# Kernel optimization log

Hardware: AMD Instinct MI355X
Metric: run time of the kernel (lower is better)

Reference implementation:

```python
import jax, jax.numpy as jnp
import numpy as np

B, T, E, H = 4, 2048, 1024, 16
HS = E // H
FF = 4 * E


def _layernorm(x, g, b, eps=1e-5):
    mu = jnp.mean(x, axis=-1, keepdims=True)
    var = jnp.var(x, axis=-1, keepdims=True)
    return (x - mu) * jax.lax.rsqrt(var + eps) * g + b


def setup_inputs() -> dict:
    key = jax.random.key(0)
    ks = jax.random.split(key, 12)
    s = E ** -0.5
    return {
        "x": jax.random.normal(ks[0], (B, T, E), jnp.float32),
        "Wq": jax.random.normal(ks[1], (E, E), jnp.float32) * s,
        "Wk": jax.random.normal(ks[2], (E, E), jnp.float32) * s,
        "Wv": jax.random.normal(ks[3], (E, E), jnp.float32) * s,
        "Wp": jax.random.normal(ks[4], (E, E), jnp.float32) * s,
        "bp": jnp.zeros((E,), jnp.float32),
        "W1": jax.random.normal(ks[5], (E, FF), jnp.float32) * s,
        "b1": jnp.zeros((FF,), jnp.float32),
        "W2": jax.random.normal(ks[6], (FF, E), jnp.float32) * (FF ** -0.5),
        "b2": jnp.zeros((E,), jnp.float32),
        "g1": jnp.ones((E,), jnp.float32),
        "be1": jnp.zeros((E,), jnp.float32),
        "g2": jnp.ones((E,), jnp.float32),
        "be2": jnp.zeros((E,), jnp.float32),
    }


def reference(x, Wq, Wk, Wv, Wp, bp, W1, b1, W2, b2, g1, be1, g2, be2):
    h = _layernorm(x, g1, be1)
    # per-head projections: Wq columns laid out head-by-head (matches concat order)
    q = (h @ Wq).reshape(B, T, H, HS).transpose(0, 2, 1, 3)  # [B,H,T,hs]
    k = (h @ Wk).reshape(B, T, H, HS).transpose(0, 2, 1, 3)
    v = (h @ Wv).reshape(B, T, H, HS).transpose(0, 2, 1, 3)
    # NOTE: original scales by full embedding size C**-0.5, not head_size
    scores = jnp.einsum("bhqd,bhkd->bhqk", q, k) * (E ** -0.5)
    causal = jnp.tril(jnp.ones((T, T), bool))
    scores = jnp.where(causal, scores, -jnp.inf)
    wei = jax.nn.softmax(scores, axis=-1)
    attn = jnp.einsum("bhqk,bhkd->bhqd", wei, v)  # [B,H,T,hs]
    attn = attn.transpose(0, 2, 1, 3).reshape(B, T, E)
    x = x + attn @ Wp + bp
    h2 = _layernorm(x, g2, be2)
    ff = jax.nn.relu(h2 @ W1 + b1) @ W2 + b2
    return x + ff
```

## Files before the change

kernel.cpp:

```cpp
#include <hip/hip_runtime.h>
#include <stdint.h>

typedef unsigned short u16;
typedef short s8v __attribute__((ext_vector_type(8)));
typedef float f32x4 __attribute__((ext_vector_type(4)));

#define B_SZ 4
#define T_SEQ 2048
#define E_DIM 1024
#define H_NUM 16
#define HS 64
#define FF_DIM 4096
#define M_ROWS 8192
#define QSCALE 0.0450842200f

__device__ __forceinline__ u16 f2bf(float f) {
    unsigned int u = __builtin_bit_cast(unsigned int, f);
    u += 0x7fffu + ((u >> 16) & 1u);
    return (u16)(u >> 16);
}

__device__ __forceinline__ void async_copy16(const void* g, void* l) {
    __builtin_amdgcn_global_load_lds(
        (const __attribute__((address_space(1))) unsigned int*)g,
        (__attribute__((address_space(3))) unsigned int*)l, 16, 0, 0);
}

__global__ __launch_bounds__(256)
void transpose_cast4(const float* __restrict__ s0, const float* __restrict__ s1,
                     const float* __restrict__ s2, const float* __restrict__ s3,
                     u16* __restrict__ dqkv, u16* __restrict__ dp) {
    __shared__ float tile[32][33];
    const int zz = blockIdx.z;
    const float* src = (zz == 0) ? s0 : (zz == 1) ? s1 : (zz == 2) ? s2 : s3;
    u16* dst = (zz < 3) ? dqkv + (size_t)zz * 1048576 : dp;
    int n0 = blockIdx.x * 32, k0 = blockIdx.y * 32;
    int tx = threadIdx.x, ty = threadIdx.y;
#pragma unroll
    for (int i = 0; i < 4; i++)
        tile[ty + i * 8][tx] = src[(size_t)(k0 + ty + i * 8) * 1024 + n0 + tx];
    __syncthreads();
#pragma unroll
    for (int i = 0; i < 4; i++)
        dst[(size_t)(n0 + ty + i * 8) * 1024 + k0 + tx] = f2bf(tile[tx][ty + i * 8]);
}

__global__ __launch_bounds__(256)
void transpose_cast(const float* __restrict__ src, u16* __restrict__ dst, int K, int N) {
    __shared__ float tile[32][33];
    int n0 = blockIdx.x * 32, k0 = blockIdx.y * 32;
    int tx = threadIdx.x, ty = threadIdx.y;
#pragma unroll
    for (int i = 0; i < 4; i++)
        tile[ty + i * 8][tx] = src[(size_t)(k0 + ty + i * 8) * N + n0 + tx];
    __syncthreads();
#pragma unroll
    for (int i = 0; i < 4; i++)
        dst[(size_t)(n0 + ty + i * 8) * K + k0 + tx] = f2bf(tile[tx][ty + i * 8]);
}

__global__ __launch_bounds__(256)
void transpose_v(const u16* __restrict__ V, u16* __restrict__ VT) {
    __shared__ u16 tile[64][80];
    const int t0 = blockIdx.x * 64;
    const size_t hoff = (size_t)blockIdx.y * (T_SEQ * HS);
    const int r = threadIdx.x >> 2, c0 = (threadIdx.x & 3) * 16;
    const u16* src = V + hoff + (size_t)(t0 + r) * HS + c0;
    *(s8v*)&tile[r][c0] = *(const s8v*)src;
    *(s8v*)&tile[r][c0 + 8] = *(const s8v*)(src + 8);
    __syncthreads();
    u16 tmp[16];
#pragma unroll
    for (int e = 0; e < 16; e++) tmp[e] = tile[c0 + e][r];
    u16* dst = VT + hoff + (size_t)r * T_SEQ + t0 + c0;
    *(s8v*)dst = *(const s8v*)&tmp[0];
    *(s8v*)(dst + 8) = *(const s8v*)&tmp[8];
}

__global__ __launch_bounds__(256)
void ln_kernel(const float* __restrict__ x, const float* __restrict__ g,
               const float* __restrict__ b, u16* __restrict__ out) {
    int row = blockIdx.x;
    int tid = threadIdx.x;
    float4 v = ((const float4*)(x + (size_t)row * E_DIM))[tid];
    float s = v.x + v.y + v.z + v.w;
    float sq = v.x * v.x + v.y * v.y + v.z * v.z + v.w * v.w;
#pragma unroll
    for (int off = 32; off; off >>= 1) {
        s += __shfl_xor(s, off);
        sq += __shfl_xor(sq, off);
    }
    __shared__ float sh[8];
    int w = tid >> 6, lane = tid & 63;
    if (lane == 0) { sh[w] = s; sh[4 + w] = sq; }
    __syncthreads();
    s = sh[0] + sh[1] + sh[2] + sh[3];
    sq = sh[4] + sh[5] + sh[6] + sh[7];
    float mu = s * (1.f / E_DIM);
    float var = sq * (1.f / E_DIM) - mu * mu;
    float rs = rsqrtf(var + 1e-5f);
    float4 gv = ((const float4*)g)[tid];
    float4 bv = ((const float4*)b)[tid];
    ushort4 o;
    o.x = f2bf((v.x - mu) * rs * gv.x + bv.x);
    o.y = f2bf((v.y - mu) * rs * gv.y + bv.y);
    o.z = f2bf((v.z - mu) * rs * gv.z + bv.z);
    o.w = f2bf((v.w - mu) * rs * gv.w + bv.w);
    ((ushort4*)(out + (size_t)row * E_DIM))[tid] = o;
}

template <int MODE>
__global__ __launch_bounds__(512)
void gemm_bt128(const u16* __restrict__ A, const u16* __restrict__ BT,
                int M, int N, int K,
                const float* __restrict__ bias, const float* __restrict__ resid,
                float* __restrict__ outf, u16* __restrict__ outb) {
    __shared__ __align__(16) u16 As[3][256 * 64];
    __shared__ __align__(16) u16 Bs[3][128 * 64];

    const int gx = gridDim.x;
    const int nwg = gx * gridDim.y;
    const int l = blockIdx.y * gx + blockIdx.x;
    const int sw = (l & 7) * (nwg >> 3) + (l >> 3);
    const int tRow = (sw / gx) * 256, tCol = (sw % gx) * 128;

    const int tid = threadIdx.x, w = tid >> 6, lane = tid & 63;
    const int wr = w >> 1, wc = w & 1, lr = lane & 15, hg = lane >> 4;
    const int nk = K >> 6;

    f32x4 z = {0.f, 0.f, 0.f, 0.f};
    f32x4 acc[4][4];
#pragma unroll
    for (int m = 0; m < 4; m++)
#pragma unroll
        for (int n = 0; n < 4; n++) acc[m][n] = z;

    auto STAGE_A = [&](int kt, int c) {
#pragma unroll
        for (int i = 0; i < 4; i++) {
            int chunk = i * 512 + tid;
            int row = chunk >> 3, j = chunk & 7;
            int js = (j ^ (row & 7)) << 3;
            async_copy16(A + (size_t)(tRow + row) * K + (kt << 6) + js,
                         &As[c][(i * 512 + w * 64) * 8]);
        }
    };
    auto STAGE_B = [&](int kt, int c) {
#pragma unroll
        for (int i = 0; i < 2; i++) {
            int chunk = i * 512 + tid;
            int row = chunk >> 3, j = chunk & 7;
            int js = (j ^ (row & 7)) << 3;
            async_copy16(BT + (size_t)(tCol + row) * K + (kt << 6) + js,
                         &Bs[c][(i * 512 + w * 64) * 8]);
        }
    };

    STAGE_A(0, 0); STAGE_B(0, 0);
    STAGE_A(1, 1); STAGE_B(1, 1);
    asm volatile("s_waitcnt vmcnt(6)" ::: "memory");
    asm volatile("s_barrier" ::: "memory");

    for (int t = 0; t < nk; ++t) {
        const int bu = t % 3, nx = (t + 2) % 3;
        const u16* Ab = &As[bu][0];
        const u16* Bb = &Bs[bu][0];
        const bool more = (t + 2 < nk);

        s8v af0[2][2], bf[4][2];
#pragma unroll
        for (int m = 0; m < 2; m++)
#pragma unroll
            for (int kk = 0; kk < 2; kk++) {
                int r = wr * 64 + m * 16 + lr;
                af0[m][kk] = *(const s8v*)&Ab[r * 64 + (((kk * 4 + hg) ^ (r & 7)) << 3)];
            }
#pragma unroll
        for (int n = 0; n < 4; n++)
#pragma unroll
            for (int kk = 0; kk < 2; kk++) {
                int r = wc * 64 + n * 16 + lr;
                bf[n][kk] = *(const s8v*)&Bb[r * 64 + (((kk * 4 + hg) ^ (r & 7)) << 3)];
            }
        if (more) STAGE_A(t + 2, nx);
        asm volatile("s_barrier" ::: "memory");
        __builtin_amdgcn_s_setprio(1);
#pragma unroll
        for (int m = 0; m < 2; m++)
#pragma unroll
            for (int n = 0; n < 4; n++)
#pragma unroll
                for (int kk = 0; kk < 2; kk++)
                    acc[m][n] = __builtin_amdgcn_mfma_f32_16x16x32_bf16(
                        af0[m][kk], bf[n][kk], acc[m][n], 0, 0, 0);
        __builtin_amdgcn_s_setprio(0);
        asm volatile("s_barrier" ::: "memory");

        s8v af1[2][2];
#pragma unroll
        for (int m = 0; m < 2; m++)
#pragma unroll
            for (int kk = 0; kk < 2; kk++) {
                int r = wr * 64 + (m + 2) * 16 + lr;
                af1[m][kk] = *(const s8v*)&Ab[r * 64 + (((kk * 4 + hg) ^ (r & 7)) << 3)];
            }
        if (more) STAGE_B(t + 2, nx);
        asm volatile("s_barrier" ::: "memory");
        __builtin_amdgcn_s_setprio(1);
#pragma unroll
        for (int m = 0; m < 2; m++)
#pragma unroll
            for (int n = 0; n < 4; n++)
#pragma unroll
                for (int kk = 0; kk < 2; kk++)
                    acc[m + 2][n] = __builtin_amdgcn_mfma_f32_16x16x32_bf16(
                        af1[m][kk], bf[n][kk], acc[m + 2][n], 0, 0, 0);
        __builtin_amdgcn_s_setprio(0);
        if (more) asm volatile("s_waitcnt vmcnt(6)" ::: "memory");
        else      asm volatile("s_waitcnt vmcnt(0)" ::: "memory");
        asm volatile("s_barrier" ::: "memory");
    }

#pragma unroll
    for (int m = 0; m < 4; m++)
#pragma unroll
        for (int n = 0; n < 4; n++)
#pragma unroll
            for (int r = 0; r < 4; r++) {
                int row = tRow + wr * 64 + m * 16 + hg * 4 + r;
                int col = tCol + wc * 64 + n * 16 + lr;
                float v = acc[m][n][r];
                if (MODE == 0) {
                    int type = col >> 10, c2 = col & 1023;
                    int h = c2 >> 6, d = c2 & 63;
                    int bb = row >> 11, tt = row & 2047;
                    if (type == 0) v *= QSCALE;
                    outb[(size_t)type * 8388608 +
                         (((size_t)(bb * H_NUM + h) * T_SEQ + tt) << 6) + d] = f2bf(v);
                } else if (MODE == 1) {
                    v += bias[col];
                    v = fmaxf(v, 0.f);
                    outb[(size_t)row * N + col] = f2bf(v);
                } else {
                    outf[(size_t)row * N + col] =
                        resid[(size_t)row * N + col] + v + bias[col];
                }
            }
}

template <int MODE>
__global__ __launch_bounds__(512)
void gemm_bt256(const u16* __restrict__ A, const u16* __restrict__ BT,
                int M, int N, int K,
                const float* __restrict__ bias, const float* __restrict__ resid,
                float* __restrict__ outf, u16* __restrict__ outb) {
    __shared__ __align__(16) u16 As[2][256 * 64];
    __shared__ __align__(16) u16 Bs[2][256 * 64];

    const int gx = gridDim.x;
    const int nwg = gx * gridDim.y;
    const int l = blockIdx.y * gx + blockIdx.x;
    const int sw = (l & 7) * (nwg >> 3) + (l >> 3);
    const int tRow = (sw / gx) * 256, tCol = (sw % gx) * 256;

    const int tid = threadIdx.x, w = tid >> 6, lane = tid & 63;
    const int wr = w >> 2, wc = w & 3, lr = lane & 15, hg = lane >> 4;
    const int nk = K >> 6;

    f32x4 z = {0.f, 0.f, 0.f, 0.f};
    f32x4 acc[8][4];
#pragma unroll
    for (int m = 0; m < 8; m++)
#pragma unroll
        for (int n = 0; n < 4; n++) acc[m][n] = z;

    auto STAGE_A = [&](int kt, int c, int h) {
#pragma unroll
        for (int i = 0; i < 2; i++) {
            int chunk = h * 1024 + i * 512 + tid;
            int row = chunk >> 3, j = chunk & 7;
            int js = (j ^ (row & 7)) << 3;
            async_copy16(A + (size_t)(tRow + row) * K + (kt << 6) + js,
                         &As[c][(h * 1024 + i * 512 + w * 64) * 8]);
        }
    };
    auto STAGE_B = [&](int kt, int c, int h) {
#pragma unroll
        for (int i = 0; i < 2; i++) {
            int chunk = h * 1024 + i * 512 + tid;
            int row = chunk >> 3, j = chunk & 7;
            int js = (j ^ (row & 7)) << 3;
            async_copy16(BT + (size_t)(tCol + row) * K + (kt << 6) + js,
                         &Bs[c][(h * 1024 + i * 512 + w * 64) * 8]);
        }
    };

    STAGE_B(0, 0, 0); STAGE_B(0, 0, 1); STAGE_A(0, 0, 0); STAGE_A(0, 0, 1);
    asm volatile("s_waitcnt vmcnt(2)" ::: "memory");
    asm volatile("s_barrier" ::: "memory");

    for (int t = 0; t < nk; ++t) {
        const int cur = t & 1, nxt = cur ^ 1;
        const u16* Ab = &As[cur][0];
        const u16* Bb = &Bs[cur][0];
        const bool more = (t + 1 < nk);

        s8v bf[4][2];
#pragma unroll
        for (int p = 0; p < 4; p++) {
            s8v af[2][2];
#pragma unroll
            for (int mm = 0; mm < 2; mm++)
#pragma unroll
                for (int kk = 0; kk < 2; kk++) {
                    int r = (2 * p + mm) * 32 + wr * 16 + lr;
                    af[mm][kk] = *(const s8v*)&Ab[r * 64 + (((kk * 4 + hg) ^ (r & 7)) << 3)];
                }
            if (p == 0) {
#pragma unroll
                for (int n = 0; n < 4; n++)
#pragma unroll
                    for (int kk = 0; kk < 2; kk++) {
                        int r = n * 64 + wc * 16 + lr;
                        bf[n][kk] = *(const s8v*)&Bb[r * 64 + (((kk * 4 + hg) ^ (r & 7)) << 3)];
                    }
            }
            if (more) {
                if (p == 0) STAGE_B(t + 1, nxt, 0);
                else if (p == 1) STAGE_B(t + 1, nxt, 1);
                else if (p == 2) STAGE_A(t + 1, nxt, 0);
                else STAGE_A(t + 1, nxt, 1);
            }
            asm volatile("s_barrier" ::: "memory");
            __builtin_amdgcn_s_setprio(1);
#pragma unroll
            for (int mm = 0; mm < 2; mm++)
#pragma unroll
                for (int n = 0; n < 4; n++)
#pragma unroll
                    for (int kk = 0; kk < 2; kk++)
                        acc[2 * p + mm][n] = __builtin_amdgcn_mfma_f32_16x16x32_bf16(
                            af[mm][kk], bf[n][kk], acc[2 * p + mm][n], 0, 0, 0);
            __builtin_amdgcn_s_setprio(0);
            if (p == 1) {
                if (more) asm volatile("s_waitcnt vmcnt(4)" ::: "memory");
                else      asm volatile("s_waitcnt vmcnt(0)" ::: "memory");
            } else if (p == 3) {
                if (more) asm volatile("s_waitcnt vmcnt(2)" ::: "memory");
                else      asm volatile("s_waitcnt vmcnt(0)" ::: "memory");
            }
            asm volatile("s_barrier" ::: "memory");
        }
    }

#pragma unroll
    for (int m = 0; m < 8; m++)
#pragma unroll
        for (int n = 0; n < 4; n++)
#pragma unroll
            for (int r = 0; r < 4; r++) {
                int row = tRow + m * 32 + wr * 16 + hg * 4 + r;
                int col = tCol + n * 64 + wc * 16 + lr;
                float v = acc[m][n][r];
                if (MODE == 1) {
                    v += bias[col];
                    v = fmaxf(v, 0.f);
                    outb[(size_t)row * N + col] = f2bf(v);
                } else {
                    outf[(size_t)row * N + col] =
                        resid[(size_t)row * N + col] + v + bias[col];
                }
            }
}

__global__ __launch_bounds__(512)
void attn_kernel(const u16* __restrict__ Q, const u16* __restrict__ K,
                 const u16* __restrict__ VT, u16* __restrict__ O) {
    __shared__ u16 Ks[2][64 * 64];
    __shared__ u16 Vs[2][64 * 64];
    __shared__ u16 Pl[8][16 * 64];
    const int bh = blockIdx.y;
    const u16* Qh = Q + (size_t)bh * T_SEQ * HS;
    const u16* Kh = K + (size_t)bh * T_SEQ * HS;
    const u16* VTh = VT + (size_t)bh * T_SEQ * HS;
    const int tid = threadIdx.x, w = tid >> 6, lane = tid & 63;
    const int lr = lane & 15, hg = lane >> 4;
    const int swz = (lr & 7) << 3;
    const int bb = bh >> 4, hh = bh & 15;
    const f32x4 z = {0.f, 0.f, 0.f, 0.f};

    for (int half = 0; half < 2; ++half) {
        const int qt = half ? (15 - blockIdx.x) : blockIdx.x;
        const int qb = qt * 128;
        const int nt = 2 * qt + 2;

        s8v qf[2];
        {
            const int qrow = qb + w * 16 + lr;
            qf[0] = *(const s8v*)(Qh + (size_t)qrow * HS + hg * 8);
            qf[1] = *(const s8v*)(Qh + (size_t)qrow * HS + 32 + hg * 8);
        }
        f32x4 o[4] = {z, z, z, z};
        float m_run[4] = {-1e30f, -1e30f, -1e30f, -1e30f};
        float l_part[4] = {0.f, 0.f, 0.f, 0.f};

        auto STAGE = [&](int t, int c) {
            int chunk = tid;
            int row = chunk >> 3, j = chunk & 7;
            int js = (j ^ (row & 7)) << 3;
            async_copy16(Kh + (size_t)t * (64 * HS) + row * HS + js, &Ks[c][w * 512]);
            async_copy16(VTh + (size_t)row * T_SEQ + t * 64 + js, &Vs[c][w * 512]);
        };

        int cur = 0;
        STAGE(0, 0);
        __syncthreads();

        for (int t = 0; t < nt; ++t) {
            if (t + 1 < nt) STAGE(t + 1, cur ^ 1);

            f32x4 s[4];
            __builtin_amdgcn_s_setprio(1);
#pragma unroll
            for (int n = 0; n < 4; n++) {
                f32x4 a = z;
#pragma unroll
                for (int kc = 0; kc < 2; kc++) {
                    s8v bfr = *(const s8v*)&Ks[cur][((n * 16 + lr) * 64 + kc * 32 + hg * 8) ^ swz];
                    a = __builtin_amdgcn_mfma_f32_16x16x32_bf16(qf[kc], bfr, a, 0, 0, 0);
                }
                s[n] = a;
            }
            __builtin_amdgcn_s_setprio(0);
            const bool diag = (t >= nt - 2);
            if (diag) {
#pragma unroll
                for (int n = 0; n < 4; n++)
#pragma unroll
                    for (int r = 0; r < 4; r++)
                        if ((t * 64 + n * 16 + lr) > (qb + w * 16 + hg * 4 + r))
                            s[n][r] = -1e30f;
            }
            float d0[4][4];
            float dm = -1e30f;
#pragma unroll
            for (int n = 0; n < 4; n++)
#pragma unroll
                for (int r = 0; r < 4; r++) {
                    d0[n][r] = s[n][r] - m_run[r];
                    dm = fmaxf(dm, d0[n][r]);
                }
            if (__any(dm > 8.f)) {
                float pm[4];
#pragma unroll
                for (int r = 0; r < 4; r++) {
                    float m0 = fmaxf(fmaxf(s[0][r], s[1][r]), fmaxf(s[2][r], s[3][r]));
                    m0 = fmaxf(m0, __shfl_xor(m0, 1));
                    m0 = fmaxf(m0, __shfl_xor(m0, 2));
                    m0 = fmaxf(m0, __shfl_xor(m0, 4));
                    m0 = fmaxf(m0, __shfl_xor(m0, 8));
                    pm[r] = m0;
                }
#pragma unroll
                for (int r = 0; r < 4; r++) {
                    float mn = fmaxf(m_run[r], pm[r]);
                    float al = __builtin_amdgcn_exp2f(m_run[r] - mn);
                    m_run[r] = mn;
                    l_part[r] *= al;
                    o[0][r] *= al; o[1][r] *= al; o[2][r] *= al; o[3][r] *= al;
                }
#pragma unroll
                for (int n = 0; n < 4; n++)
#pragma unroll
                    for (int r = 0; r < 4; r++) d0[n][r] = s[n][r] - m_run[r];
            }
#pragma unroll
            for (int n = 0; n < 4; n++)
#pragma unroll
                for (int r = 0; r < 4; r++) {
                    float p = __builtin_amdgcn_exp2f(d0[n][r]);
                    s[n][r] = p;
                    l_part[r] += p;
                }
            u16* Pw = &Pl[w][0];
#pragma unroll
            for (int n = 0; n < 4; n++)
#pragma unroll
                for (int r = 0; r < 4; r++) {
                    int prow = hg * 4 + r;
                    Pw[(prow * 64 + n * 16 + lr) ^ ((prow & 7) << 3)] = f2bf(s[n][r]);
                }
            asm volatile("s_waitcnt lgkmcnt(0)" ::: "memory");
            __builtin_amdgcn_s_setprio(1);
#pragma unroll
            for (int n = 0; n < 4; n++) {
#pragma unroll
                for (int kc = 0; kc < 2; kc++) {
                    s8v pa = *(const s8v*)&Pw[(lr * 64 + kc * 32 + hg * 8) ^ swz];
                    s8v vb = *(const s8v*)&Vs[cur][((n * 16 + lr) * 64 + kc * 32 + hg * 8) ^ swz];
                    o[n] = __builtin_amdgcn_mfma_f32_16x16x32_bf16(pa, vb, o[n], 0, 0, 0);
                }
            }
            __builtin_amdgcn_s_setprio(0);
            __syncthreads();
            cur ^= 1;
        }
        float rl[4];
#pragma unroll
        for (int r = 0; r < 4; r++) {
            float lsum = l_part[r];
            lsum += __shfl_xor(lsum, 1);
            lsum += __shfl_xor(lsum, 2);
            lsum += __shfl_xor(lsum, 4);
            lsum += __shfl_xor(lsum, 8);
            rl[r] = 1.f / lsum;
        }
#pragma unroll
        for (int n = 0; n < 4; n++)
#pragma unroll
            for (int r = 0; r < 4; r++) {
                int trow = qb + w * 16 + hg * 4 + r;
                O[((size_t)(bb * T_SEQ + trow)) * E_DIM + hh * HS + n * 16 + lr] =
                    f2bf(o[n][r] * rl[r]);
            }
    }
}

extern "C" void kernel_launch(void* const* d_in, const int* in_sizes, int n_in,
                              void* d_out, int out_size, void* d_ws, size_t ws_size,
                              hipStream_t stream) {
    (void)in_sizes; (void)n_in; (void)out_size; (void)ws_size;
    const float* x  = (const float*)d_in[0];
    const float* Wq = (const float*)d_in[1];
    const float* Wk = (const float*)d_in[2];
    const float* Wv = (const float*)d_in[3];
    const float* Wp = (const float*)d_in[4];
    const float* bp = (const float*)d_in[5];
    const float* W1 = (const float*)d_in[6];
    const float* b1 = (const float*)d_in[7];
    const float* W2 = (const float*)d_in[8];
    const float* b2 = (const float*)d_in[9];
    const float* g1  = (const float*)d_in[10];
    const float* be1 = (const float*)d_in[11];
    const float* g2  = (const float*)d_in[12];
    const float* be2 = (const float*)d_in[13];

    char* ws = (char*)d_ws;
    u16* wqkv_t  = (u16*)(ws);
    u16* wp_t    = (u16*)(ws + 6291456);
    u16* w1_t    = (u16*)(ws + 8388608);
    u16* w2_t    = (u16*)(ws + 16777216);
    u16* h_bf    = (u16*)(ws + 25165824);
    u16* q_bf    = (u16*)(ws + 41943040);
    u16* attn_bf = q_bf + 3 * 8388608;
    u16* ff1     = q_bf;
    float* x2    = (float*)(ws + 109051904);
    u16* vt_bf   = h_bf;

    dim3 b32(32, 8);
    transpose_cast4<<<dim3(32, 32, 4), b32, 0, stream>>>(Wq, Wk, Wv, Wp, wqkv_t, wp_t);
    transpose_cast<<<dim3(128, 32), b32, 0, stream>>>(W1, w1_t, 1024, 4096);
    transpose_cast<<<dim3(32, 128), b32, 0, stream>>>(W2, w2_t, 4096, 1024);

    ln_kernel<<<M_ROWS, 256, 0, stream>>>(x, g1, be1, h_bf);
    gemm_bt128<0><<<dim3(24, 32), 512, 0, stream>>>(h_bf, wqkv_t, M_ROWS, 3072, 1024,
                                                    nullptr, nullptr, nullptr, q_bf);
    transpose_v<<<dim3(32, 64), 256, 0, stream>>>(q_bf + 2 * 8388608, vt_bf);
    attn_kernel<<<dim3(8, 64), 512, 0, stream>>>(q_bf, q_bf + 8388608, vt_bf, attn_bf);
    gemm_bt128<2><<<dim3(8, 32), 512, 0, stream>>>(attn_bf, wp_t, M_ROWS, 1024, 1024,
                                                   bp, x, x2, nullptr);
    ln_kernel<<<M_ROWS, 256, 0, stream>>>(x2, g2, be2, h_bf);
    gemm_bt256<1><<<dim3(16, 32), 512, 0, stream>>>(h_bf, w1_t, M_ROWS, 4096, 1024,
                                                    b1, nullptr, nullptr, ff1);
    gemm_bt128<2><<<dim3(8, 32), 512, 0, stream>>>(ff1, w2_t, M_ROWS, 1024, 4096,
                                                   b2, x2, (float*)d_out, nullptr);
}
```

Before: 361.8 us.

## Split-K the W2 GEMM with 256-tile kernel plus reduction; merge W1/W2 casts

The FF2 GEMM (K=4096, N=1024) moves from the 128-tile kernel to the 256-tile kernel with a 2-way split over K. Each split writes bf16 partials into reused workspace, and a new elementwise kernel sums them with the residual and bias. The aim is larger tiles and more reuse while keeping enough workgroups, since a 256 tile alone gives only 128 blocks. The W1/W2 transpose-cast launches are merged into one, and attention P values are now truncated to bf16 instead of rounded. The costs are extra partial traffic and a reduction pass, and the bf16 partials and truncation lose some precision.

```diff
diff --git a/kernel.cpp b/kernel.cpp
--- a/kernel.cpp
+++ b/kernel.cpp
@@ -18,6 +18,11 @@
     unsigned int u = __builtin_bit_cast(unsigned int, f);
     u += 0x7fffu + ((u >> 16) & 1u);
     return (u16)(u >> 16);
+}
+
+__device__ __forceinline__ float bf2f(u16 u) {
+    unsigned int v = ((unsigned int)u) << 16;
+    return __builtin_bit_cast(float, v);
 }
 
 __device__ __forceinline__ void async_copy16(const void* g, void* l) {
@@ -46,9 +51,21 @@
 }
 
 __global__ __launch_bounds__(256)
-void transpose_cast(const float* __restrict__ src, u16* __restrict__ dst, int K, int N) {
+void transpose_cast_w12(const float* __restrict__ W1, const float* __restrict__ W2,
+                        u16* __restrict__ d1, u16* __restrict__ d2) {
     __shared__ float tile[32][33];
-    int n0 = blockIdx.x * 32, k0 = blockIdx.y * 32;
+    const int zz = blockIdx.z;
+    const float* src;
+    u16* dst;
+    int n0, k0, N, K;
+    if (zz == 0) {
+        src = W1; dst = d1; N = 4096; K = 1024;
+        n0 = blockIdx.x * 32; k0 = blockIdx.y * 32;
+    } else {
+        src = W2; dst = d2; N = 1024; K = 4096;
+        int idx = blockIdx.y * 128 + blockIdx.x;
+        n0 = (idx & 31) * 32; k0 = (idx >> 5) * 32;
+    }
     int tx = threadIdx.x, ty = threadIdx.y;
 #pragma unroll
     for (int i = 0; i < 4; i++)
@@ -251,7 +268,7 @@
 template <int MODE>
 __global__ __launch_bounds__(512)
 void gemm_bt256(const u16* __restrict__ A, const u16* __restrict__ BT,
-                int M, int N, int K,
+                int M, int N, int Kst, int klen,
                 const float* __restrict__ bias, const float* __restrict__ resid,
                 float* __restrict__ outf, u16* __restrict__ outb) {
     __shared__ __align__(16) u16 As[2][256 * 64];
@@ -262,10 +279,13 @@
     const int l = blockIdx.y * gx + blockIdx.x;
     const int sw = (l & 7) * (nwg >> 3) + (l >> 3);
     const int tRow = (sw / gx) * 256, tCol = (sw % gx) * 256;
+    const size_t koff = (size_t)blockIdx.z * klen;
+    const u16* Az = A + koff;
+    const u16* BTz = BT + koff;
 
     const int tid = threadIdx.x, w = tid >> 6, lane = tid & 63;
     const int wr = w >> 2, wc = w & 3, lr = lane & 15, hg = lane >> 4;
-    const int nk = K >> 6;
+    const int nk = klen >> 6;
 
     f32x4 z = {0.f, 0.f, 0.f, 0.f};
     f32x4 acc[8][4];
@@ -280,7 +300,7 @@
             int chunk = h * 1024 + i * 512 + tid;
             int row = chunk >> 3, j = chunk & 7;
             int js = (j ^ (row & 7)) << 3;
-            async_copy16(A + (size_t)(tRow + row) * K + (kt << 6) + js,
+            async_copy16(Az + (size_t)(tRow + row) * Kst + (kt << 6) + js,
                          &As[c][(h * 1024 + i * 512 + w * 64) * 8]);
         }
     };
@@ -290,7 +310,7 @@
             int chunk = h * 1024 + i * 512 + tid;
             int row = chunk >> 3, j = chunk & 7;
             int js = (j ^ (row & 7)) << 3;
-            async_copy16(BT + (size_t)(tCol + row) * K + (kt << 6) + js,
+            async_copy16(BTz + (size_t)(tCol + row) * Kst + (kt << 6) + js,
                          &Bs[c][(h * 1024 + i * 512 + w * 64) * 8]);
         }
     };
@@ -353,6 +373,8 @@
         }
     }
 
+    u16* outp = outb;
+    if (MODE == 3 && blockIdx.z == 1) outp = (u16*)outf;
 #pragma unroll
     for (int m = 0; m < 8; m++)
 #pragma unroll
@@ -365,12 +387,33 @@
                 if (MODE == 1) {
                     v += bias[col];
                     v = fmaxf(v, 0.f);
-                    outb[(size_t)row * N + col] = f2bf(v);
-                } else {
+                    outp[(size_t)row * N + col] = f2bf(v);
+                } else if (MODE == 2) {
                     outf[(size_t)row * N + col] =
                         resid[(size_t)row * N + col] + v + bias[col];
-                }
-            }
+                } else {
+                    outp[(size_t)row * N + col] = f2bf(v);
+                }
+            }
+}
+
+__global__ __launch_bounds__(256)
+void reduce_w2(const u16* __restrict__ p0, const u16* __restrict__ p1,
+               const float* __restrict__ resid, const float* __restrict__ bias,
+               float* __restrict__ out) {
+    const int total = M_ROWS * E_DIM / 4;
+    for (int i = blockIdx.x * 256 + threadIdx.x; i < total; i += gridDim.x * 256) {
+        float4 r = ((const float4*)resid)[i];
+        float4 bb = ((const float4*)bias)[i & 255];
+        ushort4 a = ((const ushort4*)p0)[i];
+        ushort4 c = ((const ushort4*)p1)[i];
+        float4 o;
+        o.x = bf2f(a.x) + bf2f(c.x) + r.x + bb.x;
+        o.y = bf2f(a.y) + bf2f(c.y) + r.y + bb.y;
+        o.z = bf2f(a.z) + bf2f(c.z) + r.z + bb.z;
+        o.w = bf2f(a.w) + bf2f(c.w) + r.w + bb.w;
+        ((float4*)out)[i] = o;
+    }
 }
 
 __global__ __launch_bounds__(512)
@@ -488,7 +531,9 @@
 #pragma unroll
                 for (int r = 0; r < 4; r++) {
                     int prow = hg * 4 + r;
-                    Pw[(prow * 64 + n * 16 + lr) ^ ((prow & 7) << 3)] = f2bf(s[n][r]);
+                    float pv = s[n][r];
+                    Pw[(prow * 64 + n * 16 + lr) ^ ((prow & 7) << 3)] =
+                        (u16)(__builtin_bit_cast(unsigned int, pv) >> 16);
                 }
             asm volatile("s_waitcnt lgkmcnt(0)" ::: "memory");
             __builtin_amdgcn_s_setprio(1);
@@ -556,11 +601,12 @@
     u16* ff1     = q_bf;
     float* x2    = (float*)(ws + 109051904);
     u16* vt_bf   = h_bf;
+    u16* part0   = (u16*)ws;
+    u16* part1   = h_bf;
 
     dim3 b32(32, 8);
     transpose_cast4<<<dim3(32, 32, 4), b32, 0, stream>>>(Wq, Wk, Wv, Wp, wqkv_t, wp_t);
-    transpose_cast<<<dim3(128, 32), b32, 0, stream>>>(W1, w1_t, 1024, 4096);
-    transpose_cast<<<dim3(32, 128), b32, 0, stream>>>(W2, w2_t, 4096, 1024);
+    transpose_cast_w12<<<dim3(128, 32, 2), b32, 0, stream>>>(W1, W2, w1_t, w2_t);
 
     ln_kernel<<<M_ROWS, 256, 0, stream>>>(x, g1, be1, h_bf);
     gemm_bt128<0><<<dim3(24, 32), 512, 0, stream>>>(h_bf, wqkv_t, M_ROWS, 3072, 1024,
@@ -570,8 +616,9 @@
     gemm_bt128<2><<<dim3(8, 32), 512, 0, stream>>>(attn_bf, wp_t, M_ROWS, 1024, 1024,
                                                    bp, x, x2, nullptr);
     ln_kernel<<<M_ROWS, 256, 0, stream>>>(x2, g2, be2, h_bf);
-    gemm_bt256<1><<<dim3(16, 32), 512, 0, stream>>>(h_bf, w1_t, M_ROWS, 4096, 1024,
+    gemm_bt256<1><<<dim3(16, 32), 512, 0, stream>>>(h_bf, w1_t, M_ROWS, 4096, 1024, 1024,
                                                     b1, nullptr, nullptr, ff1);
-    gemm_bt128<2><<<dim3(8, 32), 512, 0, stream>>>(ff1, w2_t, M_ROWS, 1024, 4096,
-                                                   b2, x2, (float*)d_out, nullptr);
-}
+    gemm_bt256<3><<<dim3(4, 32, 2), 512, 0, stream>>>(ff1, w2_t, M_ROWS, 1024, 4096, 2048,
+                                                      nullptr, nullptr, (float*)part1, part0);
+    reduce_w2<<<2048, 256, 0, stream>>>(part0, part1, x2, b2, (float*)d_out);
+}
```

New measurement: 355.0 us. No clear change (-1.9%).
